# Optimization experiments

Measured on AMD Instinct MI355X. Metric: run time of the kernel, lower is better.

Reference implementation:

```python
import jax, jax.numpy as jnp
import numpy as np

EPS = 1e-4  # softmax_kernel eps

def softmax_kernel(data, projection, is_query):
    # data: [b,h,n,d], projection: [m,d]
    d = data.shape[-1]
    m = projection.shape[0]
    data_normalizer = d ** -0.25
    ratio = m ** -0.5
    data_dash = jnp.einsum('bhnd,md->bhnm', data_normalizer * data, projection)
    diag_data = (jnp.sum(data ** 2, axis=-1) * 0.5 * data_normalizer ** 2)[..., None]  # [b,h,n,1]
    if is_query:
        stab = jnp.max(data_dash, axis=-1, keepdims=True)
    else:
        stab = jnp.max(data_dash)
    return ratio * (jnp.exp(data_dash - diag_data - stab) + EPS)

def linear_attention(q, k, v):
    # q,k: [b,h,n,m]; v: [b,h,n,e]
    k_cumsum = jnp.sum(k, axis=-2)                                  # [b,h,m]
    D_inv = 1.0 / jnp.einsum('bhnm,bhm->bhn', q, k_cumsum)          # [b,h,n]
    context = jnp.einsum('bhnm,bhne->bhme', k, v)                   # [b,h,m,e]
    return jnp.einsum('bhme,bhnm,bhn->bhne', context, q, D_inv)     # [b,h,n,e]

def setup_inputs() -> dict:
    key = jax.random.key(0)
    kq, kk, kv, kp = jax.random.split(key, 4)
    B, H, N, D = 4, 8, 4096, 64
    M = 266  # int(64 * ln(64))
    q = jax.random.normal(kq, (B, H, N, D), dtype=jnp.float32)
    k = jax.random.normal(kk, (B, H, N, D), dtype=jnp.float32)
    v = jax.random.normal(kv, (B, H, N, D), dtype=jnp.float32)
    # Gaussian random-feature projection (stand-in for orthogonal blocks; same math path)
    projection = jax.random.normal(kp, (M, D), dtype=jnp.float32)
    return {"q": q, "k": k, "v": v, "projection": projection}

def reference(q, k, v, projection):
    q_prime = softmax_kernel(q, projection, is_query=True)
    k_prime = softmax_kernel(k, projection, is_query=False)
    return linear_attention(q_prime, k_prime, v)
```

## Files before the change

### kernel.cpp

```cpp
#include <hip/hip_runtime.h>
#include <math.h>

#define BHX 32
#define NN 4096
#define DD 64
#define MM 266
#define MP 272
#define NORMZ 0.35355339059327379f
#define RATIO 0.06131393394849658f
#define EPSV 1e-4f
#define NEG_INF (-3.4e38f)
#define LSTR 72
#define GSTR 320

typedef __attribute__((ext_vector_type(8))) short bfrag;
typedef __attribute__((ext_vector_type(4))) float f32x4;

#define MFMA(a, b, c) __builtin_amdgcn_mfma_f32_16x16x32_bf16((a), (b), (c), 0, 0, 0)

__device__ inline ushort bf16rne(float x) {
    union { float f; unsigned u; } c; c.f = x;
    unsigned r = c.u + 0x7FFFu + ((c.u >> 16) & 1u);
    return (ushort)(r >> 16);
}
__device__ inline float bf2f(ushort h) {
    union { unsigned u; float f; } c; c.u = ((unsigned)h) << 16;
    return c.f;
}
__device__ inline void splitf(float x, ushort& h, ushort& l) {
    h = bf16rne(x);
    l = bf16rne(x - bf2f(h));
}

__global__ void proj_split(const float* __restrict__ proj,
                           ushort* __restrict__ pH, ushort* __restrict__ pL)
{
    int i = (blockIdx.x * 256 + threadIdx.x) * 4;
    int m = i >> 6;
    float4 x = (m < MM) ? *(const float4*)(proj + i) : make_float4(0.f, 0.f, 0.f, 0.f);
    ushort h0, l0, h1, l1, h2, l2, h3, l3;
    splitf(x.x, h0, l0); splitf(x.y, h1, l1); splitf(x.z, h2, l2); splitf(x.w, h3, l3);
    *(ushort4*)(pH + i) = make_ushort4(h0, h1, h2, h3);
    *(ushort4*)(pL + i) = make_ushort4(l0, l1, l2, l3);
}

__global__ void vsum_kernel(const float* __restrict__ v, float* __restrict__ vsum)
{
    __shared__ float red[4][64];
    const int t = threadIdx.x, hd = blockIdx.y, nc = blockIdx.x;
    const int e = t & 63, g = t >> 6;
    const float* vb = v + ((size_t)hd * NN + nc * 512) * DD;
    float s = 0.f;
    for (int j = 0; j < 128; ++j) s += vb[(j * 4 + g) * DD + e];
    red[g][e] = s;
    __syncthreads();
    if (t < 64) atomicAdd(&vsum[hd * DD + t], red[0][t] + red[1][t] + red[2][t] + red[3][t]);
}

__global__ void reduce_max_kernel(const float* __restrict__ partmax,
                                  float* __restrict__ stab, int n)
{
    __shared__ float sm[256];
    const int t = threadIdx.x;
    float mx = NEG_INF;
    for (int i = t; i < n; i += 256) mx = fmaxf(mx, partmax[i]);
    sm[t] = mx;
    __syncthreads();
    for (int s = 128; s > 0; s >>= 1) {
        if (t < s) sm[t] = fmaxf(sm[t], sm[t + s]);
        __syncthreads();
    }
    if (t == 0) *stab = sm[0];
}

__launch_bounds__(256, 2)
__global__ void kpass(const float* __restrict__ kin, const float* __restrict__ vin,
                      const ushort* __restrict__ pjH, const ushort* __restrict__ pjL,
                      float* __restrict__ ctxP, float* __restrict__ kcP,
                      float* __restrict__ pmax)
{
    __shared__ ushort dataH[64 * LSTR], dataLo[64 * LSTR];
    __shared__ ushort vTH[64 * LSTR], vTLo[64 * LSTR];
    __shared__ ushort r2H[64 * LSTR], r2Lo[64 * LSTR];
    __shared__ float diagS[64];
    __shared__ float kcS[MP];
    __shared__ float redS[4];

    const int t = threadIdx.x;
    const int w = t >> 6;
    const int lane = t & 63;
    const int l15 = lane & 15;
    const int q = lane >> 4;
    const int hd = blockIdx.y;
    const int nb = blockIdx.x;

    if (t < 256) kcS[t] = 0.f;
    if (t < 16) kcS[256 + t] = 0.f;

    const f32x4 zf = {0.f, 0.f, 0.f, 0.f};
    f32x4 cacc[4][4];
    f32x4 cacc4 = zf;
    #pragma unroll
    for (int c = 0; c < 4; ++c)
        #pragma unroll
        for (int e = 0; e < 4; ++e) cacc[c][e] = zf;
    float bmaxl = NEG_INF;

    #pragma unroll 1
    for (int st = 0; st < 4; ++st) {
        const int n0 = (nb << 8) + (st << 6);
        __syncthreads();

        const float* kb = kin + ((size_t)hd * NN + n0) * DD;
        #pragma unroll
        for (int j = 0; j < 4; ++j) {
            int i = (t + (j << 8)) << 2;
            int r = i >> 6, cc = i & 63;
            float4 x = *(const float4*)(kb + i);
            float x0 = x.x * NORMZ, x1 = x.y * NORMZ, x2 = x.z * NORMZ, x3 = x.w * NORMZ;
            ushort h0, l0, h1, l1, h2, l2, h3, l3;
            splitf(x0, h0, l0); splitf(x1, h1, l1); splitf(x2, h2, l2); splitf(x3, h3, l3);
            *(ushort4*)&dataH[r * LSTR + cc] = make_ushort4(h0, h1, h2, h3);
            *(ushort4*)&dataLo[r * LSTR + cc] = make_ushort4(l0, l1, l2, l3);
            float ss = x0 * x0 + x1 * x1 + x2 * x2 + x3 * x3;
            #pragma unroll
            for (int d = 1; d < 16; d <<= 1) ss += __shfl_xor(ss, d);
            if (l15 == 0) diagS[r] = 0.5f * ss;
        }
        const float* vb = vin + ((size_t)hd * NN + n0) * DD;
        #pragma unroll
        for (int j = 0; j < 4; ++j) {
            int i = (t + (j << 8)) << 2;
            int n = i >> 6, e = i & 63;
            float4 x = *(const float4*)(vb + i);
            ushort h, l;
            splitf(x.x, h, l); vTH[(e + 0) * LSTR + n] = h; vTLo[(e + 0) * LSTR + n] = l;
            splitf(x.y, h, l); vTH[(e + 1) * LSTR + n] = h; vTLo[(e + 1) * LSTR + n] = l;
            splitf(x.z, h, l); vTH[(e + 2) * LSTR + n] = h; vTLo[(e + 2) * LSTR + n] = l;
            splitf(x.w, h, l); vTH[(e + 3) * LSTR + n] = h; vTLo[(e + 3) * LSTR + n] = l;
        }
        __syncthreads();

        bfrag aH[2], aL[2];
        {
            const int row = (w << 4) + l15;
            aH[0] = *(const bfrag*)&dataH[row * LSTR + (q << 3)];
            aH[1] = *(const bfrag*)&dataH[row * LSTR + 32 + (q << 3)];
            aL[0] = *(const bfrag*)&dataLo[row * LSTR + (q << 3)];
            aL[1] = *(const bfrag*)&dataLo[row * LSTR + 32 + (q << 3)];
        }

        #pragma unroll
        for (int c = 0; c < 5; ++c) {
            const int mtiles = (c < 4) ? 4 : 1;
            const int m0 = c << 6;
            {
                const int tot = mtiles << 7;
                for (int idx = t; idx < tot; idx += 256) {
                    int i = idx << 3; int r = i >> 6, cc = i & 63;
                    *(uint4*)&r2H[r * LSTR + cc] = *(const uint4*)(pjH + ((m0 + r) << 6) + cc);
                    *(uint4*)&r2Lo[r * LSTR + cc] = *(const uint4*)(pjL + ((m0 + r) << 6) + cc);
                }
            }
            __syncthreads();

            f32x4 dd4[4];
            #pragma unroll
            for (int mt = 0; mt < 4; ++mt) {
                if (mt >= mtiles) break;
                const int mrow = (mt << 4) + l15;
                bfrag bH0 = *(const bfrag*)&r2H[mrow * LSTR + (q << 3)];
                bfrag bH1 = *(const bfrag*)&r2H[mrow * LSTR + 32 + (q << 3)];
                bfrag bL0 = *(const bfrag*)&r2Lo[mrow * LSTR + (q << 3)];
                bfrag bL1 = *(const bfrag*)&r2Lo[mrow * LSTR + 32 + (q << 3)];
                f32x4 a = zf;
                a = MFMA(aH[0], bL0, a);
                a = MFMA(aH[1], bL1, a);
                a = MFMA(aL[0], bH0, a);
                a = MFMA(aL[1], bH1, a);
                a = MFMA(aH[0], bH0, a);
                a = MFMA(aH[1], bH1, a);
                dd4[mt] = a;
            }
            #pragma unroll
            for (int mt = 0; mt < 4; ++mt) {
                if (mt >= mtiles) break;
                const int mg = m0 + (mt << 4) + l15;
                const bool valid = (mg < MM);
                ushort uh[4], ul[4];
                float csum = 0.f;
                #pragma unroll
                for (int reg = 0; reg < 4; ++reg) {
                    float dv = dd4[mt][reg];
                    float u = 0.f;
                    if (valid) {
                        bmaxl = fmaxf(bmaxl, dv);
                        u = __expf(dv - diagS[(w << 4) + (q << 2) + reg]);
                    }
                    csum += u;
                    splitf(u, uh[reg], ul[reg]);
                }
                *(ushort4*)&dataH[((mt << 4) + l15) * LSTR + (w << 4) + (q << 2)] =
                    make_ushort4(uh[0], uh[1], uh[2], uh[3]);
                *(ushort4*)&dataLo[((mt << 4) + l15) * LSTR + (w << 4) + (q << 2)] =
                    make_ushort4(ul[0], ul[1], ul[2], ul[3]);
                csum += __shfl_xor(csum, 16);
                csum += __shfl_xor(csum, 32);
                if (q == 0) atomicAdd(&kcS[mg], csum);
            }
            __syncthreads();

            if (c < 4) {
                const int mrow = (w << 4) + l15;
                bfrag uH0 = *(const bfrag*)&dataH[mrow * LSTR + (q << 3)];
                bfrag uH1 = *(const bfrag*)&dataH[mrow * LSTR + 32 + (q << 3)];
                bfrag uL0 = *(const bfrag*)&dataLo[mrow * LSTR + (q << 3)];
                bfrag uL1 = *(const bfrag*)&dataLo[mrow * LSTR + 32 + (q << 3)];
                #pragma unroll
                for (int et = 0; et < 4; ++et) {
                    const int erow = (et << 4) + l15;
                    bfrag vH0 = *(const bfrag*)&vTH[erow * LSTR + (q << 3)];
                    bfrag vH1 = *(const bfrag*)&vTH[erow * LSTR + 32 + (q << 3)];
                    bfrag vL0 = *(const bfrag*)&vTLo[erow * LSTR + (q << 3)];
                    bfrag vL1 = *(const bfrag*)&vTLo[erow * LSTR + 32 + (q << 3)];
                    f32x4 a = cacc[c][et];
                    a = MFMA(uH0, vL0, a);
                    a = MFMA(uH1, vL1, a);
                    a = MFMA(uL0, vH0, a);
                    a = MFMA(uL1, vH1, a);
                    a = MFMA(uH0, vH0, a);
                    a = MFMA(uH1, vH1, a);
                    cacc[c][et] = a;
                }
            } else {
                const int mrow = l15;
                bfrag uH0 = *(const bfrag*)&dataH[mrow * LSTR + (q << 3)];
                bfrag uH1 = *(const bfrag*)&dataH[mrow * LSTR + 32 + (q << 3)];
                bfrag uL0 = *(const bfrag*)&dataLo[mrow * LSTR + (q << 3)];
                bfrag uL1 = *(const bfrag*)&dataLo[mrow * LSTR + 32 + (q << 3)];
                const int erow = (w << 4) + l15;
                bfrag vH0 = *(const bfrag*)&vTH[erow * LSTR + (q << 3)];
                bfrag vH1 = *(const bfrag*)&vTH[erow * LSTR + 32 + (q << 3)];
                bfrag vL0 = *(const bfrag*)&vTLo[erow * LSTR + (q << 3)];
                bfrag vL1 = *(const bfrag*)&vTLo[erow * LSTR + 32 + (q << 3)];
                f32x4 a = cacc4;
                a = MFMA(uH0, vL0, a);
                a = MFMA(uH1, vL1, a);
                a = MFMA(uL0, vH0, a);
                a = MFMA(uL1, vH1, a);
                a = MFMA(uH0, vH0, a);
                a = MFMA(uH1, vH1, a);
                cacc4 = a;
            }
        }
    }

    __syncthreads();
    {
        float bm = bmaxl;
        #pragma unroll
        for (int d = 1; d < 64; d <<= 1) bm = fmaxf(bm, __shfl_xor(bm, d));
        if (lane == 0) redS[w] = bm;
    }
    __syncthreads();
    if (t == 0) pmax[hd * 16 + nb] = fmaxf(fmaxf(redS[0], redS[1]), fmaxf(redS[2], redS[3]));
    for (int m = t; m < MP; m += 256) kcP[(size_t)(hd * 16 + nb) * MP + m] = kcS[m];
    float* cp = ctxP + (size_t)(hd * 16 + nb) * MP * DD;
    #pragma unroll
    for (int c = 0; c < 4; ++c) {
        const int mbase = (c << 6) + (w << 4) + (q << 2);
        #pragma unroll
        for (int et = 0; et < 4; ++et)
            #pragma unroll
            for (int reg = 0; reg < 4; ++reg)
                cp[(mbase + reg) * DD + (et << 4) + l15] = cacc[c][et][reg];
    }
    #pragma unroll
    for (int reg = 0; reg < 4; ++reg)
        cp[(256 + (q << 2) + reg) * DD + (w << 4) + l15] = cacc4[reg];
}

__global__ void ctx_reduce(const float* __restrict__ ctxP, const float* __restrict__ kcP,
                           const float* __restrict__ vsum, const float* __restrict__ stabp,
                           ushort* __restrict__ gH, ushort* __restrict__ gL)
{
    __shared__ ushort hiT[64][20], loT[64][20];
    const int t = threadIdx.x, mt = blockIdx.x, hd = blockIdx.y;
    const float Asc = RATIO * __expf(-*stabp);
    const float REPS = RATIO * EPSV;
    const int e = t & 63, mq = t >> 6;
    const float vs = vsum[hd * DD + e];
    #pragma unroll
    for (int i = 0; i < 4; ++i) {
        const int ml = mq * 4 + i;
        const int m = mt * 16 + ml;
        float s = 0.f;
        for (int nbk = 0; nbk < 16; ++nbk)
            s += ctxP[((size_t)(hd * 16 + nbk) * MP + m) * DD + e];
        float val = Asc * s + REPS * vs;
        ushort h, l; splitf(val, h, l);
        hiT[e][ml] = h; loT[e][ml] = l;
    }
    __syncthreads();
    {
        const int i = t * 4, e2 = i >> 4, cc = i & 15;
        ushort4 hv = make_ushort4(hiT[e2][cc], hiT[e2][cc + 1], hiT[e2][cc + 2], hiT[e2][cc + 3]);
        ushort4 lv = make_ushort4(loT[e2][cc], loT[e2][cc + 1], loT[e2][cc + 2], loT[e2][cc + 3]);
        *(ushort4*)(gH + ((size_t)hd * 80 + e2) * GSTR + mt * 16 + cc) = hv;
        *(ushort4*)(gL + ((size_t)hd * 80 + e2) * GSTR + mt * 16 + cc) = lv;
    }
    if (t < 16) {
        const int m = mt * 16 + t;
        float s = 0.f;
        for (int nbk = 0; nbk < 16; ++nbk) s += kcP[(size_t)(hd * 16 + nbk) * MP + m];
        float val = Asc * s + ((m < MM) ? REPS * (float)NN : 0.f);
        ushort h, l; splitf(val, h, l);
        gH[((size_t)hd * 80 + 64) * GSTR + m] = h;
        gL[((size_t)hd * 80 + 64) * GSTR + m] = l;
    }
}

__launch_bounds__(256, 2)
__global__ void qpass(const float* __restrict__ qin,
                      const ushort* __restrict__ pjH, const ushort* __restrict__ pjL,
                      const ushort* __restrict__ gH, const ushort* __restrict__ gL,
                      float* __restrict__ outp)
{
    __shared__ ushort dataH[64 * LSTR], dataLo[64 * LSTR];
    __shared__ ushort r2H[64 * LSTR], r2Lo[64 * LSTR];
    __shared__ ushort cbH[80 * LSTR], cbLo[80 * LSTR];
    __shared__ float diagS[64];

    const int t = threadIdx.x;
    const int w = t >> 6;
    const int lane = t & 63;
    const int l15 = lane & 15;
    const int q = lane >> 4;
    const int hd = blockIdx.y;
    const int n0 = blockIdx.x << 6;

    const float* qb = qin + ((size_t)hd * NN + n0) * DD;
    #pragma unroll
    for (int j = 0; j < 4; ++j) {
        int i = (t + (j << 8)) << 2;
        int r = i >> 6, cc = i & 63;
        float4 x = *(const float4*)(qb + i);
        float x0 = x.x * NORMZ, x1 = x.y * NORMZ, x2 = x.z * NORMZ, x3 = x.w * NORMZ;
        ushort h0, l0, h1, l1, h2, l2, h3, l3;
        splitf(x0, h0, l0); splitf(x1, h1, l1); splitf(x2, h2, l2); splitf(x3, h3, l3);
        *(ushort4*)&dataH[r * LSTR + cc] = make_ushort4(h0, h1, h2, h3);
        *(ushort4*)&dataLo[r * LSTR + cc] = make_ushort4(l0, l1, l2, l3);
        float ss = x0 * x0 + x1 * x1 + x2 * x2 + x3 * x3;
        #pragma unroll
        for (int d = 1; d < 16; d <<= 1) ss += __shfl_xor(ss, d);
        if (l15 == 0) diagS[r] = 0.5f * ss;
    }
    __syncthreads();

    bfrag aH[2], aL[2];
    {
        const int row = (w << 4) + l15;
        aH[0] = *(const bfrag*)&dataH[row * LSTR + (q << 3)];
        aH[1] = *(const bfrag*)&dataH[row * LSTR + 32 + (q << 3)];
        aL[0] = *(const bfrag*)&dataLo[row * LSTR + (q << 3)];
        aL[1] = *(const bfrag*)&dataLo[row * LSTR + 32 + (q << 3)];
    }

    const f32x4 zf = {0.f, 0.f, 0.f, 0.f};
    f32x4 ddq[17];

    #pragma unroll
    for (int c = 0; c < 5; ++c) {
        const int mtiles = (c < 4) ? 4 : 1;
        const int m0 = c << 6;
        __syncthreads();
        {
            const int tot = mtiles << 7;
            for (int idx = t; idx < tot; idx += 256) {
                int i = idx << 3; int r = i >> 6, cc = i & 63;
                *(uint4*)&r2H[r * LSTR + cc] = *(const uint4*)(pjH + ((m0 + r) << 6) + cc);
                *(uint4*)&r2Lo[r * LSTR + cc] = *(const uint4*)(pjL + ((m0 + r) << 6) + cc);
            }
        }
        __syncthreads();
        #pragma unroll
        for (int mt = 0; mt < 4; ++mt) {
            if (mt >= mtiles) break;
            const int mrow = (mt << 4) + l15;
            bfrag bH0 = *(const bfrag*)&r2H[mrow * LSTR + (q << 3)];
            bfrag bH1 = *(const bfrag*)&r2H[mrow * LSTR + 32 + (q << 3)];
            bfrag bL0 = *(const bfrag*)&r2Lo[mrow * LSTR + (q << 3)];
            bfrag bL1 = *(const bfrag*)&r2Lo[mrow * LSTR + 32 + (q << 3)];
            f32x4 a = zf;
            a = MFMA(aH[0], bL0, a);
            a = MFMA(aH[1], bL1, a);
            a = MFMA(aL[0], bH0, a);
            a = MFMA(aL[1], bH1, a);
            a = MFMA(aH[0], bH0, a);
            a = MFMA(aH[1], bH1, a);
            ddq[c * 4 + mt] = a;
        }
    }

    float rmax[4];
    #pragma unroll
    for (int reg = 0; reg < 4; ++reg) {
        float mx = NEG_INF;
        #pragma unroll
        for (int ti = 0; ti < 17; ++ti) {
            bool valid = (ti < 16) || (l15 < 10);
            if (valid) mx = fmaxf(mx, ddq[ti][reg]);
        }
        #pragma unroll
        for (int d = 1; d < 16; d <<= 1) mx = fmaxf(mx, __shfl_xor(mx, d));
        rmax[reg] = mx;
    }
    #pragma unroll
    for (int ti = 0; ti < 17; ++ti) {
        #pragma unroll
        for (int reg = 0; reg < 4; ++reg) {
            bool valid = (ti < 16) || (l15 < 10);
            float e = 0.f;
            if (valid)
                e = RATIO * (__expf(ddq[ti][reg] - diagS[(w << 4) + (q << 2) + reg] - rmax[reg]) + EPSV);
            ddq[ti][reg] = e;
        }
    }

    f32x4 oacc[5];
    #pragma unroll
    for (int et = 0; et < 5; ++et) oacc[et] = zf;

    #pragma unroll
    for (int c = 0; c < 5; ++c) {
        const int mtiles = (c < 4) ? 4 : 1;
        __syncthreads();
        {
            for (int idx = t; idx < 640; idx += 256) {
                int i = idx << 3; int e = i >> 6, mm = i & 63;
                *(uint4*)&cbH[e * LSTR + mm] =
                    *(const uint4*)(gH + ((size_t)hd * 80 + e) * GSTR + (c << 6) + mm);
                *(uint4*)&cbLo[e * LSTR + mm] =
                    *(const uint4*)(gL + ((size_t)hd * 80 + e) * GSTR + (c << 6) + mm);
            }
        }
        #pragma unroll
        for (int mt = 0; mt < 4; ++mt) {
            if (mt >= mtiles) break;
            const int ml = (mt << 4) + l15;
            #pragma unroll
            for (int reg = 0; reg < 4; ++reg) {
                ushort h, l; splitf(ddq[c * 4 + mt][reg], h, l);
                r2H[((w << 4) + (q << 2) + reg) * LSTR + ml] = h;
                r2Lo[((w << 4) + (q << 2) + reg) * LSTR + ml] = l;
            }
        }
        if (c == 4) {
            const int rown = (w << 4) + l15;
            *(ushort4*)&r2H[rown * LSTR + 16 + (q << 2)] = make_ushort4(0, 0, 0, 0);
            *(ushort4*)&r2Lo[rown * LSTR + 16 + (q << 2)] = make_ushort4(0, 0, 0, 0);
        }
        __syncthreads();
        const int arow = (w << 4) + l15;
        bfrag pH0 = *(const bfrag*)&r2H[arow * LSTR + (q << 3)];
        bfrag pL0 = *(const bfrag*)&r2Lo[arow * LSTR + (q << 3)];
        bfrag pH1, pL1;
        if (c < 4) {
            pH1 = *(const bfrag*)&r2H[arow * LSTR + 32 + (q << 3)];
            pL1 = *(const bfrag*)&r2Lo[arow * LSTR + 32 + (q << 3)];
        }
        #pragma unroll
        for (int et = 0; et < 5; ++et) {
            const int erow = (et << 4) + l15;
            bfrag cH0 = *(const bfrag*)&cbH[erow * LSTR + (q << 3)];
            bfrag cL0 = *(const bfrag*)&cbLo[erow * LSTR + (q << 3)];
            f32x4 a = oacc[et];
            a = MFMA(pH0, cL0, a);
            a = MFMA(pL0, cH0, a);
            a = MFMA(pH0, cH0, a);
            if (c < 4) {
                bfrag cH1 = *(const bfrag*)&cbH[erow * LSTR + 32 + (q << 3)];
                bfrag cL1 = *(const bfrag*)&cbLo[erow * LSTR + 32 + (q << 3)];
                a = MFMA(pH1, cL1, a);
                a = MFMA(pL1, cH1, a);
                a = MFMA(pH1, cH1, a);
            }
            oacc[et] = a;
        }
    }

    float dinv[4];
    #pragma unroll
    for (int reg = 0; reg < 4; ++reg) {
        float den = __shfl(oacc[4][reg], lane & 48);
        dinv[reg] = 1.f / den;
    }
    float* ob = outp + ((size_t)hd * NN + n0) * DD;
    #pragma unroll
    for (int et = 0; et < 4; ++et)
        #pragma unroll
        for (int reg = 0; reg < 4; ++reg)
            ob[((w << 4) + (q << 2) + reg) * DD + (et << 4) + l15] = oacc[et][reg] * dinv[reg];
}

extern "C" void kernel_launch(void* const* d_in, const int* in_sizes, int n_in,
                              void* d_out, int out_size, void* d_ws, size_t ws_size,
                              hipStream_t stream)
{
    const float* q = (const float*)d_in[0];
    const float* k = (const float*)d_in[1];
    const float* v = (const float*)d_in[2];
    const float* proj = (const float*)d_in[3];
    float* out = (float*)d_out;
    char* ws = (char*)d_ws;

    ushort* gH = (ushort*)(ws);
    ushort* gL = (ushort*)(ws + 1638400);
    float* vsm = (float*)(ws + 3276800);
    ushort* pH = (ushort*)(ws + 3284992);
    ushort* pL = (ushort*)(ws + 3319808);
    float* ctxP = (float*)(ws + 3354624);
    float* kcP = (float*)(ws + 39006208);
    float* pmax = (float*)(ws + 39563264);
    float* stab = (float*)(ws + 39565312);

    hipMemsetAsync(ws, 0, 3284992, stream);

    proj_split<<<dim3(17), 256, 0, stream>>>(proj, pH, pL);
    vsum_kernel<<<dim3(8, 32), 256, 0, stream>>>(v, vsm);
    kpass<<<dim3(16, 32), 256, 0, stream>>>(k, v, pH, pL, ctxP, kcP, pmax);
    reduce_max_kernel<<<1, 256, 0, stream>>>(pmax, stab, 512);
    ctx_reduce<<<dim3(17, 32), 256, 0, stream>>>(ctxP, kcP, vsm, stab, gH, gL);
    qpass<<<dim3(64, 32), 256, 0, stream>>>(q, pH, pL, gH, gL, out);
}
```

Before: 279.9 us.

## Load MFMA operands directly from global, fuse vsum into kpass, compute denominator in FP32

The projection and context tiles are no longer staged through shared memory. MFMA B-fragments now load straight from global or L2, which removes several block barriers per chunk and most of the LDS footprint in kpass and qpass. The q and k A-fragments are built in registers, with the squared-norm diagonal computed by shuffles. The vsum pass is folded into kpass through atomics. The normalizer denominator is now an FP32 dot product with a separate kc vector instead of a fifth MFMA tile, so qpass can use launch bounds of 4 blocks per SM. The trade-off is redundant global loads per wave and reliance on cache hits for the projection and context data.

```diff
diff --git a/kernel.cpp b/kernel.cpp
--- a/kernel.cpp
+++ b/kernel.cpp
@@ -1,7 +1,6 @@
 #include <hip/hip_runtime.h>
 #include <math.h>
 
-#define BHX 32
 #define NN 4096
 #define DD 64
 #define MM 266
@@ -31,6 +30,17 @@
     h = bf16rne(x);
     l = bf16rne(x - bf2f(h));
 }
+__device__ inline void pack8(const float4& a, const float4& b, bfrag& H, bfrag& L) {
+    ushort h, l;
+    splitf(a.x, h, l); H[0] = (short)h; L[0] = (short)l;
+    splitf(a.y, h, l); H[1] = (short)h; L[1] = (short)l;
+    splitf(a.z, h, l); H[2] = (short)h; L[2] = (short)l;
+    splitf(a.w, h, l); H[3] = (short)h; L[3] = (short)l;
+    splitf(b.x, h, l); H[4] = (short)h; L[4] = (short)l;
+    splitf(b.y, h, l); H[5] = (short)h; L[5] = (short)l;
+    splitf(b.z, h, l); H[6] = (short)h; L[6] = (short)l;
+    splitf(b.w, h, l); H[7] = (short)h; L[7] = (short)l;
+}
 
 __global__ void proj_split(const float* __restrict__ proj,
                            ushort* __restrict__ pH, ushort* __restrict__ pL)
@@ -42,19 +52,6 @@
     splitf(x.x, h0, l0); splitf(x.y, h1, l1); splitf(x.z, h2, l2); splitf(x.w, h3, l3);
     *(ushort4*)(pH + i) = make_ushort4(h0, h1, h2, h3);
     *(ushort4*)(pL + i) = make_ushort4(l0, l1, l2, l3);
-}
-
-__global__ void vsum_kernel(const float* __restrict__ v, float* __restrict__ vsum)
-{
-    __shared__ float red[4][64];
-    const int t = threadIdx.x, hd = blockIdx.y, nc = blockIdx.x;
-    const int e = t & 63, g = t >> 6;
-    const float* vb = v + ((size_t)hd * NN + nc * 512) * DD;
-    float s = 0.f;
-    for (int j = 0; j < 128; ++j) s += vb[(j * 4 + g) * DD + e];
-    red[g][e] = s;
-    __syncthreads();
-    if (t < 64) atomicAdd(&vsum[hd * DD + t], red[0][t] + red[1][t] + red[2][t] + red[3][t]);
 }
 
 __global__ void reduce_max_kernel(const float* __restrict__ partmax,
@@ -77,12 +74,10 @@
 __global__ void kpass(const float* __restrict__ kin, const float* __restrict__ vin,
                       const ushort* __restrict__ pjH, const ushort* __restrict__ pjL,
                       float* __restrict__ ctxP, float* __restrict__ kcP,
-                      float* __restrict__ pmax)
+                      float* __restrict__ pmax, float* __restrict__ vsum)
 {
-    __shared__ ushort dataH[64 * LSTR], dataLo[64 * LSTR];
+    __shared__ ushort uTH[64 * LSTR], uTL[64 * LSTR];
     __shared__ ushort vTH[64 * LSTR], vTLo[64 * LSTR];
-    __shared__ ushort r2H[64 * LSTR], r2Lo[64 * LSTR];
-    __shared__ float diagS[64];
     __shared__ float kcS[MP];
     __shared__ float redS[4];
 
@@ -94,7 +89,7 @@
     const int hd = blockIdx.y;
     const int nb = blockIdx.x;
 
-    if (t < 256) kcS[t] = 0.f;
+    kcS[t] = 0.f;
     if (t < 16) kcS[256 + t] = 0.f;
 
     const f32x4 zf = {0.f, 0.f, 0.f, 0.f};
@@ -105,74 +100,66 @@
         #pragma unroll
         for (int e = 0; e < 4; ++e) cacc[c][e] = zf;
     float bmaxl = NEG_INF;
+    float4 vacc = make_float4(0.f, 0.f, 0.f, 0.f);
 
     #pragma unroll 1
     for (int st = 0; st < 4; ++st) {
         const int n0 = (nb << 8) + (st << 6);
         __syncthreads();
 
-        const float* kb = kin + ((size_t)hd * NN + n0) * DD;
-        #pragma unroll
-        for (int j = 0; j < 4; ++j) {
-            int i = (t + (j << 8)) << 2;
-            int r = i >> 6, cc = i & 63;
-            float4 x = *(const float4*)(kb + i);
-            float x0 = x.x * NORMZ, x1 = x.y * NORMZ, x2 = x.z * NORMZ, x3 = x.w * NORMZ;
-            ushort h0, l0, h1, l1, h2, l2, h3, l3;
-            splitf(x0, h0, l0); splitf(x1, h1, l1); splitf(x2, h2, l2); splitf(x3, h3, l3);
-            *(ushort4*)&dataH[r * LSTR + cc] = make_ushort4(h0, h1, h2, h3);
-            *(ushort4*)&dataLo[r * LSTR + cc] = make_ushort4(l0, l1, l2, l3);
-            float ss = x0 * x0 + x1 * x1 + x2 * x2 + x3 * x3;
-            #pragma unroll
-            for (int d = 1; d < 16; d <<= 1) ss += __shfl_xor(ss, d);
-            if (l15 == 0) diagS[r] = 0.5f * ss;
-        }
         const float* vb = vin + ((size_t)hd * NN + n0) * DD;
         #pragma unroll
         for (int j = 0; j < 4; ++j) {
             int i = (t + (j << 8)) << 2;
             int n = i >> 6, e = i & 63;
             float4 x = *(const float4*)(vb + i);
+            vacc.x += x.x; vacc.y += x.y; vacc.z += x.z; vacc.w += x.w;
             ushort h, l;
             splitf(x.x, h, l); vTH[(e + 0) * LSTR + n] = h; vTLo[(e + 0) * LSTR + n] = l;
             splitf(x.y, h, l); vTH[(e + 1) * LSTR + n] = h; vTLo[(e + 1) * LSTR + n] = l;
             splitf(x.z, h, l); vTH[(e + 2) * LSTR + n] = h; vTLo[(e + 2) * LSTR + n] = l;
             splitf(x.w, h, l); vTH[(e + 3) * LSTR + n] = h; vTLo[(e + 3) * LSTR + n] = l;
         }
+
+        const float* kb = kin + ((size_t)hd * NN + n0) * DD;
+        const int row = (w << 4) + l15;
+        float4 x0 = *(const float4*)(kb + (row << 6) + (q << 3));
+        float4 x1 = *(const float4*)(kb + (row << 6) + (q << 3) + 4);
+        float4 x2 = *(const float4*)(kb + (row << 6) + 32 + (q << 3));
+        float4 x3 = *(const float4*)(kb + (row << 6) + 32 + (q << 3) + 4);
+        x0.x *= NORMZ; x0.y *= NORMZ; x0.z *= NORMZ; x0.w *= NORMZ;
+        x1.x *= NORMZ; x1.y *= NORMZ; x1.z *= NORMZ; x1.w *= NORMZ;
+        x2.x *= NORMZ; x2.y *= NORMZ; x2.z *= NORMZ; x2.w *= NORMZ;
+        x3.x *= NORMZ; x3.y *= NORMZ; x3.z *= NORMZ; x3.w *= NORMZ;
+        float ss = x0.x*x0.x + x0.y*x0.y + x0.z*x0.z + x0.w*x0.w
+                 + x1.x*x1.x + x1.y*x1.y + x1.z*x1.z + x1.w*x1.w
+                 + x2.x*x2.x + x2.y*x2.y + x2.z*x2.z + x2.w*x2.w
+                 + x3.x*x3.x + x3.y*x3.y + x3.z*x3.z + x3.w*x3.w;
+        ss += __shfl_xor(ss, 16);
+        ss += __shfl_xor(ss, 32);
+        float dg[4];
+        #pragma unroll
+        for (int r = 0; r < 4; ++r) dg[r] = 0.5f * __shfl(ss, (q << 2) + r);
+        bfrag aH[2], aL[2];
+        pack8(x0, x1, aH[0], aL[0]);
+        pack8(x2, x3, aH[1], aL[1]);
         __syncthreads();
-
-        bfrag aH[2], aL[2];
-        {
-            const int row = (w << 4) + l15;
-            aH[0] = *(const bfrag*)&dataH[row * LSTR + (q << 3)];
-            aH[1] = *(const bfrag*)&dataH[row * LSTR + 32 + (q << 3)];
-            aL[0] = *(const bfrag*)&dataLo[row * LSTR + (q << 3)];
-            aL[1] = *(const bfrag*)&dataLo[row * LSTR + 32 + (q << 3)];
-        }
 
         #pragma unroll
         for (int c = 0; c < 5; ++c) {
             const int mtiles = (c < 4) ? 4 : 1;
             const int m0 = c << 6;
-            {
-                const int tot = mtiles << 7;
-                for (int idx = t; idx < tot; idx += 256) {
-                    int i = idx << 3; int r = i >> 6, cc = i & 63;
-                    *(uint4*)&r2H[r * LSTR + cc] = *(const uint4*)(pjH + ((m0 + r) << 6) + cc);
-                    *(uint4*)&r2Lo[r * LSTR + cc] = *(const uint4*)(pjL + ((m0 + r) << 6) + cc);
-                }
-            }
-            __syncthreads();
 
             f32x4 dd4[4];
             #pragma unroll
             for (int mt = 0; mt < 4; ++mt) {
                 if (mt >= mtiles) break;
-                const int mrow = (mt << 4) + l15;
-                bfrag bH0 = *(const bfrag*)&r2H[mrow * LSTR + (q << 3)];
-                bfrag bH1 = *(const bfrag*)&r2H[mrow * LSTR + 32 + (q << 3)];
-                bfrag bL0 = *(const bfrag*)&r2Lo[mrow * LSTR + (q << 3)];
-                bfrag bL1 = *(const bfrag*)&r2Lo[mrow * LSTR + 32 + (q << 3)];
+                const ushort* pbH = pjH + ((m0 + (mt << 4) + l15) << 6);
+                const ushort* pbL = pjL + ((m0 + (mt << 4) + l15) << 6);
+                bfrag bH0 = *(const bfrag*)(pbH + (q << 3));
+                bfrag bH1 = *(const bfrag*)(pbH + 32 + (q << 3));
+                bfrag bL0 = *(const bfrag*)(pbL + (q << 3));
+                bfrag bL1 = *(const bfrag*)(pbL + 32 + (q << 3));
                 f32x4 a = zf;
                 a = MFMA(aH[0], bL0, a);
                 a = MFMA(aH[1], bL1, a);
@@ -182,6 +169,8 @@
                 a = MFMA(aH[1], bH1, a);
                 dd4[mt] = a;
             }
+            __syncthreads();
+
             #pragma unroll
             for (int mt = 0; mt < 4; ++mt) {
                 if (mt >= mtiles) break;
@@ -195,14 +184,14 @@
                     float u = 0.f;
                     if (valid) {
                         bmaxl = fmaxf(bmaxl, dv);
-                        u = __expf(dv - diagS[(w << 4) + (q << 2) + reg]);
+                        u = __expf(dv - dg[reg]);
                     }
                     csum += u;
                     splitf(u, uh[reg], ul[reg]);
                 }
-                *(ushort4*)&dataH[((mt << 4) + l15) * LSTR + (w << 4) + (q << 2)] =
+                *(ushort4*)&uTH[((mt << 4) + l15) * LSTR + (w << 4) + (q << 2)] =
                     make_ushort4(uh[0], uh[1], uh[2], uh[3]);
-                *(ushort4*)&dataLo[((mt << 4) + l15) * LSTR + (w << 4) + (q << 2)] =
+                *(ushort4*)&uTL[((mt << 4) + l15) * LSTR + (w << 4) + (q << 2)] =
                     make_ushort4(ul[0], ul[1], ul[2], ul[3]);
                 csum += __shfl_xor(csum, 16);
                 csum += __shfl_xor(csum, 32);
@@ -212,10 +201,10 @@
 
             if (c < 4) {
                 const int mrow = (w << 4) + l15;
-                bfrag uH0 = *(const bfrag*)&dataH[mrow * LSTR + (q << 3)];
-                bfrag uH1 = *(const bfrag*)&dataH[mrow * LSTR + 32 + (q << 3)];
-                bfrag uL0 = *(const bfrag*)&dataLo[mrow * LSTR + (q << 3)];
-                bfrag uL1 = *(const bfrag*)&dataLo[mrow * LSTR + 32 + (q << 3)];
+                bfrag uH0 = *(const bfrag*)&uTH[mrow * LSTR + (q << 3)];
+                bfrag uH1 = *(const bfrag*)&uTH[mrow * LSTR + 32 + (q << 3)];
+                bfrag uL0 = *(const bfrag*)&uTL[mrow * LSTR + (q << 3)];
+                bfrag uL1 = *(const bfrag*)&uTL[mrow * LSTR + 32 + (q << 3)];
                 #pragma unroll
                 for (int et = 0; et < 4; ++et) {
                     const int erow = (et << 4) + l15;
@@ -234,10 +223,10 @@
                 }
             } else {
                 const int mrow = l15;
-                bfrag uH0 = *(const bfrag*)&dataH[mrow * LSTR + (q << 3)];
-                bfrag uH1 = *(const bfrag*)&dataH[mrow * LSTR + 32 + (q << 3)];
-                bfrag uL0 = *(const bfrag*)&dataLo[mrow * LSTR + (q << 3)];
-                bfrag uL1 = *(const bfrag*)&dataLo[mrow * LSTR + 32 + (q << 3)];
+                bfrag uH0 = *(const bfrag*)&uTH[mrow * LSTR + (q << 3)];
+                bfrag uH1 = *(const bfrag*)&uTH[mrow * LSTR + 32 + (q << 3)];
+                bfrag uL0 = *(const bfrag*)&uTL[mrow * LSTR + (q << 3)];
+                bfrag uL1 = *(const bfrag*)&uTL[mrow * LSTR + 32 + (q << 3)];
                 const int erow = (w << 4) + l15;
                 bfrag vH0 = *(const bfrag*)&vTH[erow * LSTR + (q << 3)];
                 bfrag vH1 = *(const bfrag*)&vTH[erow * LSTR + 32 + (q << 3)];
@@ -278,11 +267,19 @@
     #pragma unroll
     for (int reg = 0; reg < 4; ++reg)
         cp[(256 + (q << 2) + reg) * DD + (w << 4) + l15] = cacc4[reg];
+    {
+        const int e0 = (t << 2) & 63;
+        atomicAdd(&vsum[hd * DD + e0 + 0], vacc.x);
+        atomicAdd(&vsum[hd * DD + e0 + 1], vacc.y);
+        atomicAdd(&vsum[hd * DD + e0 + 2], vacc.z);
+        atomicAdd(&vsum[hd * DD + e0 + 3], vacc.w);
+    }
 }
 
 __global__ void ctx_reduce(const float* __restrict__ ctxP, const float* __restrict__ kcP,
                            const float* __restrict__ vsum, const float* __restrict__ stabp,
-                           ushort* __restrict__ gH, ushort* __restrict__ gL)
+                           ushort* __restrict__ gH, ushort* __restrict__ gL,
+                           float* __restrict__ kcF)
 {
     __shared__ ushort hiT[64][20], loT[64][20];
     const int t = threadIdx.x, mt = blockIdx.x, hd = blockIdx.y;
@@ -306,30 +303,25 @@
         const int i = t * 4, e2 = i >> 4, cc = i & 15;
         ushort4 hv = make_ushort4(hiT[e2][cc], hiT[e2][cc + 1], hiT[e2][cc + 2], hiT[e2][cc + 3]);
         ushort4 lv = make_ushort4(loT[e2][cc], loT[e2][cc + 1], loT[e2][cc + 2], loT[e2][cc + 3]);
-        *(ushort4*)(gH + ((size_t)hd * 80 + e2) * GSTR + mt * 16 + cc) = hv;
-        *(ushort4*)(gL + ((size_t)hd * 80 + e2) * GSTR + mt * 16 + cc) = lv;
+        *(ushort4*)(gH + ((size_t)hd * 64 + e2) * GSTR + mt * 16 + cc) = hv;
+        *(ushort4*)(gL + ((size_t)hd * 64 + e2) * GSTR + mt * 16 + cc) = lv;
     }
     if (t < 16) {
         const int m = mt * 16 + t;
         float s = 0.f;
         for (int nbk = 0; nbk < 16; ++nbk) s += kcP[(size_t)(hd * 16 + nbk) * MP + m];
-        float val = Asc * s + ((m < MM) ? REPS * (float)NN : 0.f);
-        ushort h, l; splitf(val, h, l);
-        gH[((size_t)hd * 80 + 64) * GSTR + m] = h;
-        gL[((size_t)hd * 80 + 64) * GSTR + m] = l;
-    }
-}
-
-__launch_bounds__(256, 2)
+        kcF[hd * MP + m] = Asc * s + ((m < MM) ? REPS * (float)NN : 0.f);
+    }
+}
+
+__launch_bounds__(256, 4)
 __global__ void qpass(const float* __restrict__ qin,
                       const ushort* __restrict__ pjH, const ushort* __restrict__ pjL,
                       const ushort* __restrict__ gH, const ushort* __restrict__ gL,
+                      const float* __restrict__ kcF,
                       float* __restrict__ outp)
 {
-    __shared__ ushort dataH[64 * LSTR], dataLo[64 * LSTR];
-    __shared__ ushort r2H[64 * LSTR], r2Lo[64 * LSTR];
-    __shared__ ushort cbH[80 * LSTR], cbLo[80 * LSTR];
-    __shared__ float diagS[64];
+    __shared__ ushort qpH[64 * LSTR], qpLo[64 * LSTR];
 
     const int t = threadIdx.x;
     const int w = t >> 6;
@@ -340,31 +332,27 @@
     const int n0 = blockIdx.x << 6;
 
     const float* qb = qin + ((size_t)hd * NN + n0) * DD;
-    #pragma unroll
-    for (int j = 0; j < 4; ++j) {
-        int i = (t + (j << 8)) << 2;
-        int r = i >> 6, cc = i & 63;
-        float4 x = *(const float4*)(qb + i);
-        float x0 = x.x * NORMZ, x1 = x.y * NORMZ, x2 = x.z * NORMZ, x3 = x.w * NORMZ;
-        ushort h0, l0, h1, l1, h2, l2, h3, l3;
-        splitf(x0, h0, l0); splitf(x1, h1, l1); splitf(x2, h2, l2); splitf(x3, h3, l3);
-        *(ushort4*)&dataH[r * LSTR + cc] = make_ushort4(h0, h1, h2, h3);
-        *(ushort4*)&dataLo[r * LSTR + cc] = make_ushort4(l0, l1, l2, l3);
-        float ss = x0 * x0 + x1 * x1 + x2 * x2 + x3 * x3;
-        #pragma unroll
-        for (int d = 1; d < 16; d <<= 1) ss += __shfl_xor(ss, d);
-        if (l15 == 0) diagS[r] = 0.5f * ss;
-    }
-    __syncthreads();
-
+    const int row = (w << 4) + l15;
+    float4 x0 = *(const float4*)(qb + (row << 6) + (q << 3));
+    float4 x1 = *(const float4*)(qb + (row << 6) + (q << 3) + 4);
+    float4 x2 = *(const float4*)(qb + (row << 6) + 32 + (q << 3));
+    float4 x3 = *(const float4*)(qb + (row << 6) + 32 + (q << 3) + 4);
+    x0.x *= NORMZ; x0.y *= NORMZ; x0.z *= NORMZ; x0.w *= NORMZ;
+    x1.x *= NORMZ; x1.y *= NORMZ; x1.z *= NORMZ; x1.w *= NORMZ;
+    x2.x *= NORMZ; x2.y *= NORMZ; x2.z *= NORMZ; x2.w *= NORMZ;
+    x3.x *= NORMZ; x3.y *= NORMZ; x3.z *= NORMZ; x3.w *= NORMZ;
+    float ss = x0.x*x0.x + x0.y*x0.y + x0.z*x0.z + x0.w*x0.w
+             + x1.x*x1.x + x1.y*x1.y + x1.z*x1.z + x1.w*x1.w
+             + x2.x*x2.x + x2.y*x2.y + x2.z*x2.z + x2.w*x2.w
+             + x3.x*x3.x + x3.y*x3.y + x3.z*x3.z + x3.w*x3.w;
+    ss += __shfl_xor(ss, 16);
+    ss += __shfl_xor(ss, 32);
+    float dg[4];
+    #pragma unroll
+    for (int r = 0; r < 4; ++r) dg[r] = 0.5f * __shfl(ss, (q << 2) + r);
     bfrag aH[2], aL[2];
-    {
-        const int row = (w << 4) + l15;
-        aH[0] = *(const bfrag*)&dataH[row * LSTR + (q << 3)];
-        aH[1] = *(const bfrag*)&dataH[row * LSTR + 32 + (q << 3)];
-        aL[0] = *(const bfrag*)&dataLo[row * LSTR + (q << 3)];
-        aL[1] = *(const bfrag*)&dataLo[row * LSTR + 32 + (q << 3)];
-    }
+    pack8(x0, x1, aH[0], aL[0]);
+    pack8(x2, x3, aH[1], aL[1]);
 
     const f32x4 zf = {0.f, 0.f, 0.f, 0.f};
     f32x4 ddq[17];
@@ -373,24 +361,15 @@
     for (int c = 0; c < 5; ++c) {
         const int mtiles = (c < 4) ? 4 : 1;
         const int m0 = c << 6;
-        __syncthreads();
-        {
-            const int tot = mtiles << 7;
-            for (int idx = t; idx < tot; idx += 256) {
-                int i = idx << 3; int r = i >> 6, cc = i & 63;
-                *(uint4*)&r2H[r * LSTR + cc] = *(const uint4*)(pjH + ((m0 + r) << 6) + cc);
-                *(uint4*)&r2Lo[r * LSTR + cc] = *(const uint4*)(pjL + ((m0 + r) << 6) + cc);
-            }
-        }
-        __syncthreads();
         #pragma unroll
         for (int mt = 0; mt < 4; ++mt) {
             if (mt >= mtiles) break;
-            const int mrow = (mt << 4) + l15;
-            bfrag bH0 = *(const bfrag*)&r2H[mrow * LSTR + (q << 3)];
-            bfrag bH1 = *(const bfrag*)&r2H[mrow * LSTR + 32 + (q << 3)];
-            bfrag bL0 = *(const bfrag*)&r2Lo[mrow * LSTR + (q << 3)];
-            bfrag bL1 = *(const bfrag*)&r2Lo[mrow * LSTR + 32 + (q << 3)];
+            const ushort* pbH = pjH + ((m0 + (mt << 4) + l15) << 6);
+            const ushort* pbL = pjL + ((m0 + (mt << 4) + l15) << 6);
+            bfrag bH0 = *(const bfrag*)(pbH + (q << 3));
+            bfrag bH1 = *(const bfrag*)(pbH + 32 + (q << 3));
+            bfrag bL0 = *(const bfrag*)(pbL + (q << 3));
+            bfrag bL1 = *(const bfrag*)(pbL + 32 + (q << 3));
             f32x4 a = zf;
             a = MFMA(aH[0], bL0, a);
             a = MFMA(aH[1], bL1, a);
@@ -422,28 +401,36 @@
             bool valid = (ti < 16) || (l15 < 10);
             float e = 0.f;
             if (valid)
-                e = RATIO * (__expf(ddq[ti][reg] - diagS[(w << 4) + (q << 2) + reg] - rmax[reg]) + EPSV);
+                e = RATIO * (__expf(ddq[ti][reg] - dg[reg] - rmax[reg]) + EPSV);
             ddq[ti][reg] = e;
         }
     }
-
-    f32x4 oacc[5];
-    #pragma unroll
-    for (int et = 0; et < 5; ++et) oacc[et] = zf;
+    float dinv[4];
+    {
+        const float* kcb = kcF + hd * MP;
+        float den[4] = {0.f, 0.f, 0.f, 0.f};
+        #pragma unroll
+        for (int ti = 0; ti < 17; ++ti) {
+            float kv = kcb[(ti << 4) + l15];
+            #pragma unroll
+            for (int reg = 0; reg < 4; ++reg) den[reg] += ddq[ti][reg] * kv;
+        }
+        #pragma unroll
+        for (int reg = 0; reg < 4; ++reg) {
+            #pragma unroll
+            for (int d = 1; d < 16; d <<= 1) den[reg] += __shfl_xor(den[reg], d);
+            dinv[reg] = 1.f / den[reg];
+        }
+    }
+
+    f32x4 oacc[4];
+    #pragma unroll
+    for (int et = 0; et < 4; ++et) oacc[et] = zf;
 
     #pragma unroll
     for (int c = 0; c < 5; ++c) {
         const int mtiles = (c < 4) ? 4 : 1;
         __syncthreads();
-        {
-            for (int idx = t; idx < 640; idx += 256) {
-                int i = idx << 3; int e = i >> 6, mm = i & 63;
-                *(uint4*)&cbH[e * LSTR + mm] =
-                    *(const uint4*)(gH + ((size_t)hd * 80 + e) * GSTR + (c << 6) + mm);
-                *(uint4*)&cbLo[e * LSTR + mm] =
-                    *(const uint4*)(gL + ((size_t)hd * 80 + e) * GSTR + (c << 6) + mm);
-            }
-        }
         #pragma unroll
         for (int mt = 0; mt < 4; ++mt) {
             if (mt >= mtiles) break;
@@ -451,36 +438,37 @@
             #pragma unroll
             for (int reg = 0; reg < 4; ++reg) {
                 ushort h, l; splitf(ddq[c * 4 + mt][reg], h, l);
-                r2H[((w << 4) + (q << 2) + reg) * LSTR + ml] = h;
-                r2Lo[((w << 4) + (q << 2) + reg) * LSTR + ml] = l;
+                qpH[((w << 4) + (q << 2) + reg) * LSTR + ml] = h;
+                qpLo[((w << 4) + (q << 2) + reg) * LSTR + ml] = l;
             }
         }
         if (c == 4) {
             const int rown = (w << 4) + l15;
-            *(ushort4*)&r2H[rown * LSTR + 16 + (q << 2)] = make_ushort4(0, 0, 0, 0);
-            *(ushort4*)&r2Lo[rown * LSTR + 16 + (q << 2)] = make_ushort4(0, 0, 0, 0);
+            *(ushort4*)&qpH[rown * LSTR + 16 + (q << 2)] = make_ushort4(0, 0, 0, 0);
+            *(ushort4*)&qpLo[rown * LSTR + 16 + (q << 2)] = make_ushort4(0, 0, 0, 0);
         }
         __syncthreads();
         const int arow = (w << 4) + l15;
-        bfrag pH0 = *(const bfrag*)&r2H[arow * LSTR + (q << 3)];
-        bfrag pL0 = *(const bfrag*)&r2Lo[arow * LSTR + (q << 3)];
+        bfrag pH0 = *(const bfrag*)&qpH[arow * LSTR + (q << 3)];
+        bfrag pL0 = *(const bfrag*)&qpLo[arow * LSTR + (q << 3)];
         bfrag pH1, pL1;
         if (c < 4) {
-            pH1 = *(const bfrag*)&r2H[arow * LSTR + 32 + (q << 3)];
-            pL1 = *(const bfrag*)&r2Lo[arow * LSTR + 32 + (q << 3)];
-        }
-        #pragma unroll
-        for (int et = 0; et < 5; ++et) {
-            const int erow = (et << 4) + l15;
-            bfrag cH0 = *(const bfrag*)&cbH[erow * LSTR + (q << 3)];
-            bfrag cL0 = *(const bfrag*)&cbLo[erow * LSTR + (q << 3)];
+            pH1 = *(const bfrag*)&qpH[arow * LSTR + 32 + (q << 3)];
+            pL1 = *(const bfrag*)&qpLo[arow * LSTR + 32 + (q << 3)];
+        }
+        #pragma unroll
+        for (int et = 0; et < 4; ++et) {
+            const ushort* gbH = gH + ((size_t)hd * 64 + (et << 4) + l15) * GSTR + (c << 6);
+            const ushort* gbL = gL + ((size_t)hd * 64 + (et << 4) + l15) * GSTR + (c << 6);
+            bfrag cH0 = *(const bfrag*)(gbH + (q << 3));
+            bfrag cL0 = *(const bfrag*)(gbL + (q << 3));
             f32x4 a = oacc[et];
             a = MFMA(pH0, cL0, a);
             a = MFMA(pL0, cH0, a);
             a = MFMA(pH0, cH0, a);
             if (c < 4) {
-                bfrag cH1 = *(const bfrag*)&cbH[erow * LSTR + 32 + (q << 3)];
-                bfrag cL1 = *(const bfrag*)&cbLo[erow * LSTR + 32 + (q << 3)];
+                bfrag cH1 = *(const bfrag*)(gbH + 32 + (q << 3));
+                bfrag cL1 = *(const bfrag*)(gbL + 32 + (q << 3));
                 a = MFMA(pH1, cL1, a);
                 a = MFMA(pL1, cH1, a);
                 a = MFMA(pH1, cH1, a);
@@ -489,12 +477,6 @@
         }
     }
 
-    float dinv[4];
-    #pragma unroll
-    for (int reg = 0; reg < 4; ++reg) {
-        float den = __shfl(oacc[4][reg], lane & 48);
-        dinv[reg] = 1.f / den;
-    }
     float* ob = outp + ((size_t)hd * NN + n0) * DD;
     #pragma unroll
     for (int et = 0; et < 4; ++et)
@@ -514,22 +496,22 @@
     float* out = (float*)d_out;
     char* ws = (char*)d_ws;
 
-    ushort* gH = (ushort*)(ws);
-    ushort* gL = (ushort*)(ws + 1638400);
-    float* vsm = (float*)(ws + 3276800);
-    ushort* pH = (ushort*)(ws + 3284992);
-    ushort* pL = (ushort*)(ws + 3319808);
-    float* ctxP = (float*)(ws + 3354624);
-    float* kcP = (float*)(ws + 39006208);
-    float* pmax = (float*)(ws + 39563264);
-    float* stab = (float*)(ws + 39565312);
-
-    hipMemsetAsync(ws, 0, 3284992, stream);
+    ushort* gH  = (ushort*)(ws);
+    ushort* gL  = (ushort*)(ws + 1310720);
+    float*  vsm = (float*)(ws + 2621440);
+    ushort* pH  = (ushort*)(ws + 2629632);
+    ushort* pL  = (ushort*)(ws + 2664448);
+    float*  kcF = (float*)(ws + 2699264);
+    float*  ctxP= (float*)(ws + 2734080);
+    float*  kcP = (float*)(ws + 38385664);
+    float*  pmax= (float*)(ws + 38942720);
+    float*  stab= (float*)(ws + 38944768);
+
+    hipMemsetAsync(ws, 0, 2629632, stream);
 
     proj_split<<<dim3(17), 256, 0, stream>>>(proj, pH, pL);
-    vsum_kernel<<<dim3(8, 32), 256, 0, stream>>>(v, vsm);
-    kpass<<<dim3(16, 32), 256, 0, stream>>>(k, v, pH, pL, ctxP, kcP, pmax);
+    kpass<<<dim3(16, 32), 256, 0, stream>>>(k, v, pH, pL, ctxP, kcP, pmax, vsm);
     reduce_max_kernel<<<1, 256, 0, stream>>>(pmax, stab, 512);
-    ctx_reduce<<<dim3(17, 32), 256, 0, stream>>>(ctxP, kcP, vsm, stab, gH, gL);
-    qpass<<<dim3(64, 32), 256, 0, stream>>>(q, pH, pL, gH, gL, out);
-}
+    ctx_reduce<<<dim3(17, 32), 256, 0, stream>>>(ctxP, kcP, vsm, stab, gH, gL, kcF);
+    qpass<<<dim3(64, 32), 256, 0, stream>>>(q, pH, pL, gH, gL, kcF, out);
+}
```

Result: slower. 439.8 us (+57.1%).
